# Optimization experiments

Measured on AMD Instinct MI355X. Metric: run time of the kernel, lower is better.

Reference implementation:

```python
import jax, jax.numpy as jnp
import numpy as np

NUM_HEADS = 6
EPS = 1e-05


def setup_inputs() -> dict:
    key = jax.random.key(0)
    k1, k2, k3 = jax.random.split(key, 3)
    B, N, C = 8, 1024, 384
    x = jax.random.normal(k1, (B, N, C), dtype=jnp.float32)
    Wqkv = jax.random.normal(k2, (3 * C, C), dtype=jnp.float32) * (1.0 / np.sqrt(C))
    Wproj = jax.random.normal(k3, (C, C), dtype=jnp.float32) * (1.0 / np.sqrt(C))
    bproj = jnp.zeros((C,), dtype=jnp.float32)
    alpha = jnp.ones((1, NUM_HEADS, 1, 1), dtype=jnp.float32)
    return {"x": x, "Wqkv": Wqkv, "Wproj": Wproj, "bproj": bproj, "alpha": alpha}


def reference(x, Wqkv, Wproj, bproj, alpha):
    B, N, C = x.shape
    H = NUM_HEADS
    hd = C // H
    scale = hd ** -0.5
    # qkv projection (torch Linear: x @ W^T), split into q,k,v of shape [B,H,N,hd]
    qkv = (x @ Wqkv.T).reshape(B, N, 3, H, hd).transpose(2, 0, 3, 1, 4)
    q, k, v = qkv[0], qkv[1], qkv[2]
    attn = jnp.einsum('bhqd,bhkd->bhqk', q, k) * scale  # [B,H,N,N]
    scalattn = attn / N  # divide by attn.size(3) == N
    a = jax.nn.relu(attn)
    a = a / (jnp.sum(a, axis=-1, keepdims=True) + EPS)
    attn = alpha * a + (1.0 - alpha) * scalattn
    out = jnp.einsum('bhqk,bhkd->bhqd', attn, v)  # [B,H,N,hd]
    out = out.transpose(0, 2, 1, 3).reshape(B, N, C)
    return out @ Wproj.T + bproj
```

## Files before the change

kernel.cpp:

```cpp
#include <hip/hip_runtime.h>
#include <stdint.h>

typedef _Float16 f16;
typedef _Float16 half8 __attribute__((ext_vector_type(8)));
typedef float f32x4 __attribute__((ext_vector_type(4)));

#define MFMA16(A, B, C) __builtin_amdgcn_mfma_f32_16x16x32_f16(A, B, C, 0, 0, 0)

#define GLOAD16(g, l) __builtin_amdgcn_global_load_lds( \
    (const __attribute__((address_space(1))) uint32_t*)(g), \
    (__attribute__((address_space(3))) uint32_t*)(l), 16, 0, 0)

__device__ inline uint32_t packh(f16 a, f16 b) {
    union { f16 h[2]; uint32_t u; } t;
    t.h[0] = a; t.h[1] = b;
    return t.u;
}

union V8 { f16 h[8]; uint4 u; };

__global__ __launch_bounds__(256) void qkv_gemm(
    const float* __restrict__ x, const float* __restrict__ wq,
    f16* __restrict__ q_, f16* __restrict__ k_, f16* __restrict__ vt_) {
    __shared__ f16 sA[2][4096], sB[2][4096];
    const int tid = threadIdx.x;
    const int w = tid >> 6, lane = tid & 63;
    const int g = lane >> 4, q = lane & 15;
    const int m0 = blockIdx.x * 128, j0 = blockIdx.y * 128;
    const int wm = (w >> 1) * 64, wn = (w & 1) * 64;
    const bool isV = (j0 >= 768);

    const float* src = (w < 2) ? (x + (size_t)(m0 + w * 64) * 384)
                               : (wq + (size_t)(j0 + (w & 1) * 64) * 384);
    const int rowbase = (w & 1) * 64;

    float4 ld[8];
    auto LOADS = [&](int ks) {
#pragma unroll
        for (int r = 0; r < 4; ++r) {
            const int fidx = r * 64 + lane;
            const int row = fidx >> 2, colg = (fidx & 3) * 8;
            const float* p = src + (size_t)row * 384 + ks * 32 + colg;
            ld[2 * r]     = *(const float4*)p;
            ld[2 * r + 1] = *(const float4*)(p + 4);
        }
    };
    auto WRITE = [&](int buf) {
        f16* d = (w < 2) ? sA[buf] : sB[buf];
#pragma unroll
        for (int r = 0; r < 4; ++r) {
            const int fidx = r * 64 + lane;
            const int row = rowbase + (fidx >> 2);
            const int ch = (fidx & 3) ^ ((row & 6) >> 1);
            V8 H;
            float vv[8] = {ld[2*r].x, ld[2*r].y, ld[2*r].z, ld[2*r].w,
                           ld[2*r+1].x, ld[2*r+1].y, ld[2*r+1].z, ld[2*r+1].w};
#pragma unroll
            for (int j = 0; j < 8; ++j) H.h[j] = (f16)vv[j];
            *(uint4*)&d[row * 32 + ch * 8] = H.u;
        }
    };

    f32x4 acc[4][4];
#pragma unroll
    for (int i = 0; i < 4; ++i)
#pragma unroll
        for (int j = 0; j < 4; ++j) acc[i][j] = (f32x4){0.f, 0.f, 0.f, 0.f};

    LOADS(0);
    WRITE(0);
    asm volatile("s_waitcnt lgkmcnt(0)" ::: "memory");
    __builtin_amdgcn_s_barrier();

    int cur = 0;
    for (int ks = 0; ks < 12; ++ks) {
        if (ks < 11) LOADS(ks + 1);

        half8 am[4], bn[4];
#pragma unroll
        for (int mi = 0; mi < 4; ++mi) {
            const int row = wm + 16 * mi + q;
            const int ch = (g ^ ((row & 6) >> 1)) * 8;
            am[mi] = *(const half8*)&sA[cur][row * 32 + ch];
        }
#pragma unroll
        for (int nj = 0; nj < 4; ++nj) {
            const int row = wn + 16 * nj + q;
            const int ch = (g ^ ((row & 6) >> 1)) * 8;
            bn[nj] = *(const half8*)&sB[cur][row * 32 + ch];
        }
        if (!isV) {
#pragma unroll
            for (int mi = 0; mi < 4; ++mi)
#pragma unroll
                for (int nj = 0; nj < 4; ++nj)
                    acc[mi][nj] = MFMA16(bn[nj], am[mi], acc[mi][nj]);
        } else {
#pragma unroll
            for (int mi = 0; mi < 4; ++mi)
#pragma unroll
                for (int nj = 0; nj < 4; ++nj)
                    acc[mi][nj] = MFMA16(am[mi], bn[nj], acc[mi][nj]);
        }
        if (ks < 11) {
            WRITE(cur ^ 1);
            asm volatile("s_waitcnt lgkmcnt(0)" ::: "memory");
            __builtin_amdgcn_s_barrier();
            cur ^= 1;
        }
    }

    if (!isV) {
        const int t = j0 / 384;
        const float sc = (t == 0) ? 0.125f : 1.0f;
        f16* dst = (t == 0) ? q_ : k_;
#pragma unroll
        for (int nj = 0; nj < 4; ++nj) {
            const int jb = j0 + wn + 16 * nj + 4 * g;
            const int h = (jb - t * 384) >> 6, d0 = jb & 63;
#pragma unroll
            for (int mi = 0; mi < 4; ++mi) {
                const int mg = m0 + wm + 16 * mi + q;
                const int b = mg >> 10, n = mg & 1023;
                const size_t base = (size_t)(b * 6 + h) * 65536 + (size_t)n * 64 + d0;
                union { f16 x[4]; uint2 u; } H;
#pragma unroll
                for (int r = 0; r < 4; ++r) H.x[r] = (f16)(acc[mi][nj][r] * sc);
                *(uint2*)&dst[base] = H.u;
            }
        }
    } else {
#pragma unroll
        for (int nj = 0; nj < 4; ++nj) {
            const int jc = j0 + wn + 16 * nj + q;
            const int h = (jc - 768) >> 6, d = jc & 63;
#pragma unroll
            for (int mi = 0; mi < 4; ++mi) {
                const int mg = m0 + wm + 16 * mi + 4 * g;
                const int b = mg >> 10, n = mg & 1023;
                const size_t bh = (size_t)(b * 6 + h);
                union { f16 x[4]; uint2 u; } HV;
#pragma unroll
                for (int r = 0; r < 4; ++r) HV.x[r] = (f16)acc[mi][nj][r];
                *(uint2*)&vt_[bh * 65536 + (size_t)d * 1024 + n] = HV.u;
            }
        }
    }
}

__global__ __launch_bounds__(256) void attn_mfma(
    const f16* __restrict__ q_, const f16* __restrict__ k_,
    const f16* __restrict__ vt_, const float* __restrict__ alpha,
    f16* __restrict__ ao_) {
    __shared__ f16 sK[2][4096], sV[2][4096];
    const int tid = threadIdx.x;
    const int w = tid >> 6, lane = tid & 63;
    const int g = lane >> 4, q = lane & 15;
    const int bh = blockIdx.x % 48, h = bh % 6;
    const int n0 = (blockIdx.x / 48) * 64;

    const size_t kbb = (size_t)bh * 131072;
    const int rl8 = lane >> 3, cl8 = lane & 7;

    auto STAGE = [&](int buf, int kt) {
        const size_t kb = kbb + (size_t)kt * 8192;
        const size_t vb = kbb + (size_t)kt * 128;
#pragma unroll
        for (int i2 = 0; i2 < 2; ++i2) {
            const int rloc = 16 * w + i2 * 8 + rl8;
            const int chs = (cl8 ^ (rloc & 7)) << 4;
            const int ldso = (16 * w + i2 * 8) * 64;
            GLOAD16((const char*)k_ + kb + (size_t)rloc * 128 + chs, &sK[buf][ldso]);
            GLOAD16((const char*)vt_ + vb + (size_t)rloc * 2048 + chs, &sV[buf][ldso]);
        }
    };

    const size_t qbase = (size_t)bh * 65536 + (size_t)(n0 + 16 * w + q) * 64;
    half8 Qh[2];
    Qh[0] = *(const half8*)&q_[qbase + g * 8];
    Qh[1] = *(const half8*)&q_[qbase + 32 + g * 8];
    const float al = alpha[h];
    const float cg = (1.0f - al) * (1.0f / 1024.0f);
    const bool useLin = (cg != 0.0f);

    f32x4 accP[4], accS[4];
#pragma unroll
    for (int i = 0; i < 4; ++i) {
        accP[i] = (f32x4){0.f, 0.f, 0.f, 0.f};
        accS[i] = (f32x4){0.f, 0.f, 0.f, 0.f};
    }
    float rs = 0.f;

    asm volatile("" ::: "memory");
    STAGE(0, 0);
    int cur = 0;
    for (int kt = 0; kt < 16; ++kt) {
        __builtin_amdgcn_s_barrier();
        if (kt < 15) {
            STAGE(cur ^ 1, kt + 1);
            asm volatile("s_waitcnt vmcnt(4)" ::: "memory");
        } else {
            asm volatile("s_waitcnt vmcnt(0)" ::: "memory");
        }
        __builtin_amdgcn_s_barrier();

        f32x4 sv[4];
        __builtin_amdgcn_s_setprio(1);
#pragma unroll
        for (int s = 0; s < 4; ++s) {
            f32x4 sa = (f32x4){0.f, 0.f, 0.f, 0.f};
            const int row = 16 * s + q;
#pragma unroll
            for (int k2 = 0; k2 < 2; ++k2) {
                const int ch = ((k2 * 4 + g) ^ (row & 7)) * 8;
                half8 kf = *(const half8*)&sK[cur][row * 64 + ch];
                sa = MFMA16(kf, Qh[k2], sa);
            }
            sv[s] = sa;
        }
        __builtin_amdgcn_s_setprio(0);

        uint32_t pk[4][2];
#pragma unroll
        for (int s = 0; s < 4; ++s) {
            float p0 = fmaxf(sv[s][0], 0.f), p1 = fmaxf(sv[s][1], 0.f);
            float p2 = fmaxf(sv[s][2], 0.f), p3 = fmaxf(sv[s][3], 0.f);
            rs += (p0 + p1) + (p2 + p3);
            pk[s][0] = packh((f16)p0, (f16)p1);
            pk[s][1] = packh((f16)p2, (f16)p3);
        }

#pragma unroll
        for (int t2 = 0; t2 < 2; ++t2) {
            union { uint32_t u[4]; half8 v; } fh;
#pragma unroll
            for (int r = 0; r < 4; ++r) {
                const int srcl = ((2 * g + (r >> 1)) & 3) * 16 + q;
                uint32_t a0 = __shfl(pk[2 * t2][r & 1], srcl, 64);
                uint32_t b0 = __shfl(pk[2 * t2 + 1][r & 1], srcl, 64);
                fh.u[r] = (g < 2) ? a0 : b0;
            }
            __builtin_amdgcn_s_setprio(1);
#pragma unroll
            for (int ds = 0; ds < 4; ++ds) {
                const int row = 16 * ds + q;
                const int ch = ((t2 * 4 + g) ^ (row & 7)) * 8;
                half8 vf = *(const half8*)&sV[cur][row * 64 + ch];
                accP[ds] = MFMA16(vf, fh.v, accP[ds]);
            }
            __builtin_amdgcn_s_setprio(0);
        }

        if (useLin) {
            uint32_t sk[4][2];
#pragma unroll
            for (int s = 0; s < 4; ++s) {
                sk[s][0] = packh((f16)sv[s][0], (f16)sv[s][1]);
                sk[s][1] = packh((f16)sv[s][2], (f16)sv[s][3]);
            }
#pragma unroll
            for (int t2 = 0; t2 < 2; ++t2) {
                union { uint32_t u[4]; half8 v; } fh;
#pragma unroll
                for (int r = 0; r < 4; ++r) {
                    const int srcl = ((2 * g + (r >> 1)) & 3) * 16 + q;
                    uint32_t a0 = __shfl(sk[2 * t2][r & 1], srcl, 64);
                    uint32_t b0 = __shfl(sk[2 * t2 + 1][r & 1], srcl, 64);
                    fh.u[r] = (g < 2) ? a0 : b0;
                }
#pragma unroll
                for (int ds = 0; ds < 4; ++ds) {
                    const int row = 16 * ds + q;
                    const int ch = ((t2 * 4 + g) ^ (row & 7)) * 8;
                    half8 vf = *(const half8*)&sV[cur][row * 64 + ch];
                    accS[ds] = MFMA16(vf, fh.v, accS[ds]);
                }
            }
        }
        cur ^= 1;
    }

    rs += __shfl_xor(rs, 16, 64);
    rs += __shfl_xor(rs, 32, 64);
    const float inv = al / (rs + 1e-5f);

    const int b = bh / 6;
    const size_t arow = (size_t)(b * 1024 + n0 + 16 * w + q) * 384 + h * 64;
#pragma unroll
    for (int ds = 0; ds < 4; ++ds) {
        const int d0 = 16 * ds + 4 * g;
        union { f16 x[4]; uint2 u; } H;
#pragma unroll
        for (int r = 0; r < 4; ++r)
            H.x[r] = (f16)(accP[ds][r] * inv + cg * accS[ds][r]);
        *(uint2*)&ao_[arow + d0] = H.u;
    }
}

__global__ __launch_bounds__(256) void proj_gemm(
    const f16* __restrict__ a_, const float* __restrict__ wp,
    const float* __restrict__ bias, float* __restrict__ out) {
    __shared__ f16 sA[2][2048], sB[2][4096];
    const int tid = threadIdx.x;
    const int w = tid >> 6, lane = tid & 63;
    const int g = lane >> 4, q = lane & 15;
    const int m0 = blockIdx.x * 64, j0 = blockIdx.y * 128;
    const int wm = (w >> 1) * 32, wn = (w & 1) * 64;

    const f16* asrc = a_ + (size_t)(m0 + w * 32) * 384;
    const float* wsrc = wp + (size_t)(j0 + (w & 1) * 64) * 384;

    uint4 lda[2];
    float4 ldw[8];
    auto LOADS = [&](int ks) {
        if (w < 2) {
#pragma unroll
            for (int r = 0; r < 2; ++r) {
                const int cidx = r * 64 + lane;
                const int row = cidx >> 2, c16 = cidx & 3;
                lda[r] = *(const uint4*)&asrc[(size_t)row * 384 + ks * 32 + c16 * 8];
            }
        } else {
#pragma unroll
            for (int r = 0; r < 4; ++r) {
                const int fidx = r * 64 + lane;
                const int row = fidx >> 2, colg = (fidx & 3) * 8;
                const float* p = wsrc + (size_t)row * 384 + ks * 32 + colg;
                ldw[2 * r]     = *(const float4*)p;
                ldw[2 * r + 1] = *(const float4*)(p + 4);
            }
        }
    };
    auto WRITE = [&](int buf) {
        if (w < 2) {
#pragma unroll
            for (int r = 0; r < 2; ++r) {
                const int cidx = r * 64 + lane;
                const int row = w * 32 + (cidx >> 2);
                const int ch = (cidx & 3) ^ ((row & 6) >> 1);
                *(uint4*)&sA[buf][row * 32 + ch * 8] = lda[r];
            }
        } else {
            const int rowbase = (w & 1) * 64;
#pragma unroll
            for (int r = 0; r < 4; ++r) {
                const int fidx = r * 64 + lane;
                const int row = rowbase + (fidx >> 2);
                const int ch = (fidx & 3) ^ ((row & 6) >> 1);
                V8 H;
                float vv[8] = {ldw[2*r].x, ldw[2*r].y, ldw[2*r].z, ldw[2*r].w,
                               ldw[2*r+1].x, ldw[2*r+1].y, ldw[2*r+1].z, ldw[2*r+1].w};
#pragma unroll
                for (int j = 0; j < 8; ++j) H.h[j] = (f16)vv[j];
                *(uint4*)&sB[buf][row * 32 + ch * 8] = H.u;
            }
        }
    };

    f32x4 acc[2][4];
#pragma unroll
    for (int i = 0; i < 2; ++i)
#pragma unroll
        for (int j = 0; j < 4; ++j) acc[i][j] = (f32x4){0.f, 0.f, 0.f, 0.f};

    LOADS(0);
    WRITE(0);
    asm volatile("s_waitcnt lgkmcnt(0)" ::: "memory");
    __builtin_amdgcn_s_barrier();

    int cur = 0;
    for (int ks = 0; ks < 12; ++ks) {
        if (ks < 11) LOADS(ks + 1);

        half8 am[2], bn[4];
#pragma unroll
        for (int mi = 0; mi < 2; ++mi) {
            const int row = wm + 16 * mi + q;
            const int ch = (g ^ ((row & 6) >> 1)) * 8;
            am[mi] = *(const half8*)&sA[cur][row * 32 + ch];
        }
#pragma unroll
        for (int nj = 0; nj < 4; ++nj) {
            const int row = wn + 16 * nj + q;
            const int ch = (g ^ ((row & 6) >> 1)) * 8;
            bn[nj] = *(const half8*)&sB[cur][row * 32 + ch];
        }
#pragma unroll
        for (int mi = 0; mi < 2; ++mi)
#pragma unroll
            for (int nj = 0; nj < 4; ++nj)
                acc[mi][nj] = MFMA16(bn[nj], am[mi], acc[mi][nj]);

        if (ks < 11) {
            WRITE(cur ^ 1);
            asm volatile("s_waitcnt lgkmcnt(0)" ::: "memory");
            __builtin_amdgcn_s_barrier();
            cur ^= 1;
        }
    }

#pragma unroll
    for (int nj = 0; nj < 4; ++nj) {
        const int jb = j0 + wn + 16 * nj + 4 * g;
        const float4 bb = *(const float4*)&bias[jb];
#pragma unroll
        for (int mi = 0; mi < 2; ++mi) {
            const int m = m0 + wm + 16 * mi + q;
            float4 o;
            o.x = acc[mi][nj][0] + bb.x;
            o.y = acc[mi][nj][1] + bb.y;
            o.z = acc[mi][nj][2] + bb.z;
            o.w = acc[mi][nj][3] + bb.w;
            *(float4*)&out[(size_t)m * 384 + jb] = o;
        }
    }
}

extern "C" void kernel_launch(void* const* d_in, const int* in_sizes, int n_in,
                              void* d_out, int out_size, void* d_ws, size_t ws_size,
                              hipStream_t stream) {
    const float* x     = (const float*)d_in[0];
    const float* Wqkv  = (const float*)d_in[1];
    const float* Wproj = (const float*)d_in[2];
    const float* bproj = (const float*)d_in[3];
    const float* alpha = (const float*)d_in[4];
    float* out = (float*)d_out;

    f16* ws = (f16*)d_ws;
    const size_t QE = 48 * 1024 * 64;

    f16* qv = ws;
    f16* kv = qv + QE;
    f16* vt = kv + QE;
    f16* ao = vt + QE;

    qkv_gemm<<<dim3(64, 9), 256, 0, stream>>>(x, Wqkv, qv, kv, vt);
    attn_mfma<<<768, 256, 0, stream>>>(qv, kv, vt, alpha, ao);
    proj_gemm<<<dim3(128, 3), 256, 0, stream>>>(ao, Wproj, bproj, out);
}
```

Baseline: 146.4 us.

## Pre-convert inputs to fp16 and pipeline GEMM staging with direct-to-LDS loads

```diff
diff --git a/kernel.cpp b/kernel.cpp
--- a/kernel.cpp
+++ b/kernel.cpp
@@ -17,12 +17,36 @@
     return t.u;
 }
 
-union V8 { f16 h[8]; uint4 u; };
+#define XE4 786432
+#define WQ4 110592
+#define WP4 36864
+
+__global__ void convert_all(const float* __restrict__ x,
+                            const float* __restrict__ wq,
+                            const float* __restrict__ wp,
+                            f16* __restrict__ xo, f16* __restrict__ wqo,
+                            f16* __restrict__ wpo) {
+    const int total = XE4 + WQ4 + WP4;
+    for (int i = blockIdx.x * blockDim.x + threadIdx.x; i < total;
+         i += gridDim.x * blockDim.x) {
+        const float* src;
+        f16* dst;
+        int idx = i;
+        if (idx < XE4) { src = x; dst = xo; }
+        else if (idx < XE4 + WQ4) { idx -= XE4; src = wq; dst = wqo; }
+        else { idx -= XE4 + WQ4; src = wp; dst = wpo; }
+        float4 v = ((const float4*)src)[idx];
+        union { f16 x[4]; uint2 u; } H;
+        H.x[0] = (f16)v.x; H.x[1] = (f16)v.y;
+        H.x[2] = (f16)v.z; H.x[3] = (f16)v.w;
+        ((uint2*)dst)[idx] = H.u;
+    }
+}
 
 __global__ __launch_bounds__(256) void qkv_gemm(
-    const float* __restrict__ x, const float* __restrict__ wq,
+    const f16* __restrict__ x16, const f16* __restrict__ w16,
     f16* __restrict__ q_, f16* __restrict__ k_, f16* __restrict__ vt_) {
-    __shared__ f16 sA[2][4096], sB[2][4096];
+    __shared__ f16 sA[3][4096], sB[3][4096];
     const int tid = threadIdx.x;
     const int w = tid >> 6, lane = tid & 63;
     const int g = lane >> 4, q = lane & 15;
@@ -30,36 +54,18 @@
     const int wm = (w >> 1) * 64, wn = (w & 1) * 64;
     const bool isV = (j0 >= 768);
 
-    const float* src = (w < 2) ? (x + (size_t)(m0 + w * 64) * 384)
-                               : (wq + (size_t)(j0 + (w & 1) * 64) * 384);
-    const int rowbase = (w & 1) * 64;
-
-    float4 ld[8];
-    auto LOADS = [&](int ks) {
-#pragma unroll
-        for (int r = 0; r < 4; ++r) {
-            const int fidx = r * 64 + lane;
-            const int row = fidx >> 2, colg = (fidx & 3) * 8;
-            const float* p = src + (size_t)row * 384 + ks * 32 + colg;
-            ld[2 * r]     = *(const float4*)p;
-            ld[2 * r + 1] = *(const float4*)(p + 4);
+    const char* gA = (const char*)x16 + (size_t)m0 * 768;
+    const char* gB = (const char*)w16 + (size_t)j0 * 768;
+    auto STAGE = [&](int buf, int ks) {
+#pragma unroll
+        for (int i = 0; i < 2; ++i) {
+            const int r0 = 32 * w + i * 16;
+            const int row = r0 + (lane >> 2);
+            const int chs = ((lane & 3) ^ ((row & 6) >> 1)) << 4;
+            GLOAD16(gA + (size_t)row * 768 + ks * 64 + chs, &sA[buf][r0 * 32]);
+            GLOAD16(gB + (size_t)row * 768 + ks * 64 + chs, &sB[buf][r0 * 32]);
         }
     };
-    auto WRITE = [&](int buf) {
-        f16* d = (w < 2) ? sA[buf] : sB[buf];
-#pragma unroll
-        for (int r = 0; r < 4; ++r) {
-            const int fidx = r * 64 + lane;
-            const int row = rowbase + (fidx >> 2);
-            const int ch = (fidx & 3) ^ ((row & 6) >> 1);
-            V8 H;
-            float vv[8] = {ld[2*r].x, ld[2*r].y, ld[2*r].z, ld[2*r].w,
-                           ld[2*r+1].x, ld[2*r+1].y, ld[2*r+1].z, ld[2*r+1].w};
-#pragma unroll
-            for (int j = 0; j < 8; ++j) H.h[j] = (f16)vv[j];
-            *(uint4*)&d[row * 32 + ch * 8] = H.u;
-        }
-    };
 
     f32x4 acc[4][4];
 #pragma unroll
@@ -67,14 +73,21 @@
 #pragma unroll
         for (int j = 0; j < 4; ++j) acc[i][j] = (f32x4){0.f, 0.f, 0.f, 0.f};
 
-    LOADS(0);
-    WRITE(0);
-    asm volatile("s_waitcnt lgkmcnt(0)" ::: "memory");
-    __builtin_amdgcn_s_barrier();
-
-    int cur = 0;
+    asm volatile("" ::: "memory");
+    STAGE(0, 0);
+    STAGE(1, 1);
     for (int ks = 0; ks < 12; ++ks) {
-        if (ks < 11) LOADS(ks + 1);
+        const int cur = ks % 3;
+        __builtin_amdgcn_s_barrier();
+        if (ks < 10) {
+            STAGE((ks + 2) % 3, ks + 2);
+            asm volatile("s_waitcnt vmcnt(8)" ::: "memory");
+        } else if (ks == 10) {
+            asm volatile("s_waitcnt vmcnt(4)" ::: "memory");
+        } else {
+            asm volatile("s_waitcnt vmcnt(0)" ::: "memory");
+        }
+        __builtin_amdgcn_s_barrier();
 
         half8 am[4], bn[4];
 #pragma unroll
@@ -89,6 +102,7 @@
             const int ch = (g ^ ((row & 6) >> 1)) * 8;
             bn[nj] = *(const half8*)&sB[cur][row * 32 + ch];
         }
+        __builtin_amdgcn_s_setprio(1);
         if (!isV) {
 #pragma unroll
             for (int mi = 0; mi < 4; ++mi)
@@ -102,12 +116,7 @@
                 for (int nj = 0; nj < 4; ++nj)
                     acc[mi][nj] = MFMA16(am[mi], bn[nj], acc[mi][nj]);
         }
-        if (ks < 11) {
-            WRITE(cur ^ 1);
-            asm volatile("s_waitcnt lgkmcnt(0)" ::: "memory");
-            __builtin_amdgcn_s_barrier();
-            cur ^= 1;
-        }
+        __builtin_amdgcn_s_setprio(0);
     }
 
     if (!isV) {
@@ -298,79 +307,54 @@
 }
 
 __global__ __launch_bounds__(256) void proj_gemm(
-    const f16* __restrict__ a_, const float* __restrict__ wp,
+    const f16* __restrict__ a_, const f16* __restrict__ wp16,
     const float* __restrict__ bias, float* __restrict__ out) {
-    __shared__ f16 sA[2][2048], sB[2][4096];
+    __shared__ f16 sA[3][2048], sB[3][4096];
     const int tid = threadIdx.x;
     const int w = tid >> 6, lane = tid & 63;
     const int g = lane >> 4, q = lane & 15;
     const int m0 = blockIdx.x * 64, j0 = blockIdx.y * 128;
     const int wm = (w >> 1) * 32, wn = (w & 1) * 64;
 
-    const f16* asrc = a_ + (size_t)(m0 + w * 32) * 384;
-    const float* wsrc = wp + (size_t)(j0 + (w & 1) * 64) * 384;
-
-    uint4 lda[2];
-    float4 ldw[8];
-    auto LOADS = [&](int ks) {
-        if (w < 2) {
-#pragma unroll
-            for (int r = 0; r < 2; ++r) {
-                const int cidx = r * 64 + lane;
-                const int row = cidx >> 2, c16 = cidx & 3;
-                lda[r] = *(const uint4*)&asrc[(size_t)row * 384 + ks * 32 + c16 * 8];
-            }
+    const char* gA = (const char*)a_ + (size_t)m0 * 768;
+    const char* gB = (const char*)wp16 + (size_t)j0 * 768;
+    auto STAGE = [&](int buf, int ks) {
+        {
+            const int r0 = 16 * w;
+            const int row = r0 + (lane >> 2);
+            const int chs = ((lane & 3) ^ ((row & 6) >> 1)) << 4;
+            GLOAD16(gA + (size_t)row * 768 + ks * 64 + chs, &sA[buf][r0 * 32]);
+        }
+#pragma unroll
+        for (int i = 0; i < 2; ++i) {
+            const int r0 = 32 * w + i * 16;
+            const int row = r0 + (lane >> 2);
+            const int chs = ((lane & 3) ^ ((row & 6) >> 1)) << 4;
+            GLOAD16(gB + (size_t)row * 768 + ks * 64 + chs, &sB[buf][r0 * 32]);
+        }
+    };
+
+    f32x4 acc[2][4];
+#pragma unroll
+    for (int i = 0; i < 2; ++i)
+#pragma unroll
+        for (int j = 0; j < 4; ++j) acc[i][j] = (f32x4){0.f, 0.f, 0.f, 0.f};
+
+    asm volatile("" ::: "memory");
+    STAGE(0, 0);
+    STAGE(1, 1);
+    for (int ks = 0; ks < 12; ++ks) {
+        const int cur = ks % 3;
+        __builtin_amdgcn_s_barrier();
+        if (ks < 10) {
+            STAGE((ks + 2) % 3, ks + 2);
+            asm volatile("s_waitcnt vmcnt(6)" ::: "memory");
+        } else if (ks == 10) {
+            asm volatile("s_waitcnt vmcnt(3)" ::: "memory");
         } else {
-#pragma unroll
-            for (int r = 0; r < 4; ++r) {
-                const int fidx = r * 64 + lane;
-                const int row = fidx >> 2, colg = (fidx & 3) * 8;
-                const float* p = wsrc + (size_t)row * 384 + ks * 32 + colg;
-                ldw[2 * r]     = *(const float4*)p;
-                ldw[2 * r + 1] = *(const float4*)(p + 4);
-            }
-        }
-    };
-    auto WRITE = [&](int buf) {
-        if (w < 2) {
-#pragma unroll
-            for (int r = 0; r < 2; ++r) {
-                const int cidx = r * 64 + lane;
-                const int row = w * 32 + (cidx >> 2);
-                const int ch = (cidx & 3) ^ ((row & 6) >> 1);
-                *(uint4*)&sA[buf][row * 32 + ch * 8] = lda[r];
-            }
-        } else {
-            const int rowbase = (w & 1) * 64;
-#pragma unroll
-            for (int r = 0; r < 4; ++r) {
-                const int fidx = r * 64 + lane;
-                const int row = rowbase + (fidx >> 2);
-                const int ch = (fidx & 3) ^ ((row & 6) >> 1);
-                V8 H;
-                float vv[8] = {ldw[2*r].x, ldw[2*r].y, ldw[2*r].z, ldw[2*r].w,
-                               ldw[2*r+1].x, ldw[2*r+1].y, ldw[2*r+1].z, ldw[2*r+1].w};
-#pragma unroll
-                for (int j = 0; j < 8; ++j) H.h[j] = (f16)vv[j];
-                *(uint4*)&sB[buf][row * 32 + ch * 8] = H.u;
-            }
-        }
-    };
-
-    f32x4 acc[2][4];
-#pragma unroll
-    for (int i = 0; i < 2; ++i)
-#pragma unroll
-        for (int j = 0; j < 4; ++j) acc[i][j] = (f32x4){0.f, 0.f, 0.f, 0.f};
-
-    LOADS(0);
-    WRITE(0);
-    asm volatile("s_waitcnt lgkmcnt(0)" ::: "memory");
-    __builtin_amdgcn_s_barrier();
-
-    int cur = 0;
-    for (int ks = 0; ks < 12; ++ks) {
-        if (ks < 11) LOADS(ks + 1);
+            asm volatile("s_waitcnt vmcnt(0)" ::: "memory");
+        }
+        __builtin_amdgcn_s_barrier();
 
         half8 am[2], bn[4];
 #pragma unroll
@@ -385,18 +369,13 @@
             const int ch = (g ^ ((row & 6) >> 1)) * 8;
             bn[nj] = *(const half8*)&sB[cur][row * 32 + ch];
         }
+        __builtin_amdgcn_s_setprio(1);
 #pragma unroll
         for (int mi = 0; mi < 2; ++mi)
 #pragma unroll
             for (int nj = 0; nj < 4; ++nj)
                 acc[mi][nj] = MFMA16(bn[nj], am[mi], acc[mi][nj]);
-
-        if (ks < 11) {
-            WRITE(cur ^ 1);
-            asm volatile("s_waitcnt lgkmcnt(0)" ::: "memory");
-            __builtin_amdgcn_s_barrier();
-            cur ^= 1;
-        }
+        __builtin_amdgcn_s_setprio(0);
     }
 
 #pragma unroll
@@ -427,14 +406,18 @@
     float* out = (float*)d_out;
 
     f16* ws = (f16*)d_ws;
+    const size_t XE = 8192 * 384;
+    const size_t WQ = 1152 * 384;
+    const size_t WP = 384 * 384;
     const size_t QE = 48 * 1024 * 64;
 
-    f16* qv = ws;
-    f16* kv = qv + QE;
-    f16* vt = kv + QE;
-    f16* ao = vt + QE;
-
-    qkv_gemm<<<dim3(64, 9), 256, 0, stream>>>(x, Wqkv, qv, kv, vt);
+    f16* x16  = ws;            f16* wq16 = x16 + XE;
+    f16* wp16 = wq16 + WQ;
+    f16* qv   = wp16 + WP;     f16* kv   = qv + QE;
+    f16* vt   = kv + QE;       f16* ao   = vt + QE;
+
+    convert_all<<<1024, 256, 0, stream>>>(x, Wqkv, Wproj, x16, wq16, wp16);
+    qkv_gemm<<<dim3(64, 9), 256, 0, stream>>>(x16, wq16, qv, kv, vt);
     attn_mfma<<<768, 256, 0, stream>>>(qv, kv, vt, alpha, ao);
-    proj_gemm<<<dim3(128, 3), 256, 0, stream>>>(ao, Wproj, bproj, out);
-}
+    proj_gemm<<<dim3(128, 3), 256, 0, stream>>>(ao, wp16, bproj, out);
+}
```

Result: faster. 133.6 us (-8.8%).
